# Kernel tuning notes

Measured on AMD Instinct MI355X. Metric: run time of the kernel, lower is better.

The kernel has to match this reference:

```python
import jax, jax.numpy as jnp
import numpy as np

M = 0.25
GAMMA = 256.0
HARD_W = 2.0
O_P = 1.0 + M
O_N = -M
DELTA_P = 1.0 - M
DELTA_N = M
NEG_BIG = -1e30  # masked-out fill for logsumexp (finite to keep grads NaN-free)


def setup_inputs() -> dict:
    key = jax.random.key(0)
    k1, k2 = jax.random.split(key)
    inputs = jax.random.normal(k1, (4096, 512), dtype=jnp.float32)
    targets = jax.random.randint(k2, (4096,), 0, 64, dtype=jnp.int64)
    return {"inputs": inputs, "targets": targets}


def reference(inputs, targets):
    n = inputs.shape[0]
    x = inputs / jnp.linalg.norm(inputs, axis=1, keepdims=True)  # L2 normalize
    sim = x @ x.T                                                # [n, n]

    same = targets[:, None] == targets[None, :]
    eye = jnp.eye(n, dtype=bool)
    pos_mask = same & ~eye
    neg_mask = ~same
    npos = pos_mask.sum(axis=1)
    nneg = neg_mask.sum(axis=1)

    sim_d = jax.lax.stop_gradient(sim)  # alphas are detached in the original
    alpha_p = jax.nn.relu(O_P - sim_d)
    alpha_n = jax.nn.relu(sim_d - O_N)

    # hard mining: scale alpha at hardest positive (min sim) / hardest negative (max sim)
    idx = jnp.arange(n)
    hard_p = jnp.argmin(jnp.where(pos_mask, sim_d, jnp.inf), axis=1)
    hard_n = jnp.argmax(jnp.where(neg_mask, sim_d, -jnp.inf), axis=1)
    hit_p = (idx[None, :] == hard_p[:, None]) & (npos > 1)[:, None]
    hit_n = (idx[None, :] == hard_n[:, None]) & (nneg > 1)[:, None]
    alpha_p = alpha_p * jnp.where(hit_p, HARD_W, 1.0)
    alpha_n = alpha_n * jnp.where(hit_n, HARD_W, 1.0)

    pos_term = jnp.where(pos_mask, -GAMMA * alpha_p * (sim - DELTA_P), NEG_BIG)
    neg_term = jnp.where(neg_mask, GAMMA * alpha_n * (sim - DELTA_N), NEG_BIG)
    lse_p = jax.nn.logsumexp(pos_term, axis=1)
    lse_n = jax.nn.logsumexp(neg_term, axis=1)

    valid = (npos > 0) & (nneg > 0)
    per_row = jnp.where(valid, jax.nn.softplus(lse_p + lse_n), 0.0)
    n_valid = jnp.maximum(valid.sum(), 1)
    return per_row.sum() / n_valid.astype(per_row.dtype)
```

## Files before the change

kernel.cpp:

```cpp
#include <hip/hip_runtime.h>


#define GAMMA_ 256.0f
#define MASKT_  (-1.0e4f)
#define MINITP_ (-1.0e4f)
#define MASKP_  (-3.0e4f)

constexpr int N_ = 4096;
constexpr int D_ = 512;
constexpr int AST_ = 520;
constexpr int CCH_ = 16;

typedef __bf16 bf16x8 __attribute__((ext_vector_type(8)));
typedef float  f32x4  __attribute__((ext_vector_type(4)));
typedef const unsigned int __attribute__((address_space(1)))* gp_t;
typedef unsigned int       __attribute__((address_space(3)))* lp_t;

__device__ __forceinline__ float pos_q(float s) {
    float d = s - 1.0f;
    return fmaf(d * d, 256.0f, -16.0f);
}
__device__ __forceinline__ float neg_q(float s) {
    float q = fmaf(s * s, 256.0f, -16.0f);
    return (s >= -0.25f) ? q : 0.0f;
}
__device__ __forceinline__ void lse_merge(float m2, float S2, float& m, float& S) {
    float mm = fmaxf(m, m2);
    S = S * __expf(m - mm) + S2 * __expf(m2 - mm);
    m = mm;
}
__device__ __forceinline__ unsigned short f2bf(float f) {
    unsigned int u = __float_as_uint(f);
    unsigned int r = u + 0x7FFFu + ((u >> 16) & 1u);
    return (unsigned short)(r >> 16);
}

__global__ __launch_bounds__(256) void k_norm(const float* __restrict__ in,
                                              unsigned short* __restrict__ xb,
                                              float* __restrict__ acc) {
    const int row  = blockIdx.x * 4 + (threadIdx.x >> 6);
    const int lane = threadIdx.x & 63;
    const float4* src = (const float4*)(in + (size_t)row * D_) + lane * 2;
    float4 a = src[0], b = src[1];
    float ss = a.x*a.x + a.y*a.y + a.z*a.z + a.w*a.w
             + b.x*b.x + b.y*b.y + b.z*b.z + b.w*b.w;
    #pragma unroll
    for (int d = 32; d >= 1; d >>= 1) ss += __shfl_xor(ss, d);
    float rn = 1.0f / sqrtf(ss);
    float v[8] = {a.x, a.y, a.z, a.w, b.x, b.y, b.z, b.w};
    union { uint4 u; unsigned short us[8]; } pk;
    #pragma unroll
    for (int k = 0; k < 8; ++k) pk.us[k] = f2bf(v[k] * rn);
    *((uint4*)(xb + (size_t)row * D_) + lane) = pk.u;
    if (blockIdx.x == 0 && threadIdx.x < 4) acc[threadIdx.x] = 0.0f;
}

__global__ __launch_bounds__(256, 4) void k_mainG(const unsigned short* __restrict__ xb,
                                                  const int* __restrict__ tg,
                                                  float* __restrict__ part) {
    constexpr int NST = 16;
    __shared__ __align__(16) unsigned short Bs[2][16][AST_];

    const int tid  = threadIdx.x;
    const int wave = tid >> 6, lane = tid & 63;
    const int n16  = lane & 15, quad = lane >> 4;
    const int rg   = (int)blockIdx.x >> 4;
    const int cc   = (int)blockIdx.x & 15;
    const int rowBase = rg * 64 + wave * 16;
    const int colBase = cc * 256;

    bf16x8 af[16];
    {
        const bf16x8* ap = (const bf16x8*)(xb + (size_t)(rowBase + n16) * D_ + quad * 8);
        #pragma unroll
        for (int kk = 0; kk < 16; ++kk) af[kk] = ap[kk * 4];
    }
    int tr[4];
    #pragma unroll
    for (int r = 0; r < 4; ++r) tr[r] = tg[rowBase + quad * 4 + r];

    float m_p[4], S_p[4], m_n[4], S_n[4], mxn[4];
    #pragma unroll
    for (int r = 0; r < 4; ++r) {
        m_p[r] = MINITP_; S_p[r] = 0.f; m_n[r] = 0.f; S_n[r] = 0.f; mxn[r] = -2.0f;
    }

    const char* gstage = (const char*)xb + (size_t)colBase * 1024 + lane * 16;

    #pragma unroll
    for (int p = 0; p < 4; ++p) {
        int j = p * 4 + wave;
        __builtin_amdgcn_global_load_lds((gp_t)(const void*)(gstage + j * 1024),
                                         (lp_t)(void*)&Bs[0][j][0], 16, 0, 0);
    }
    int tc_cur = tg[colBase + n16];

    auto epi = [&](const f32x4& a0, const f32x4& a1, int tcv, bool withDiag) {
        #pragma unroll
        for (int r = 0; r < 4; ++r) {
            float sim = a0[r] + a1[r];
            bool samec = (tr[r] == tcv);
            float u = samec ? (sim - 1.0f) : sim;
            float t = fmaf(u * u, 256.0f, -16.0f);
            if (!samec && sim < -0.25f) t = 0.0f;
            if (withDiag && n16 == quad * 4 + r) t = MASKP_;
            float ms = samec ? m_p[r] : m_n[r];
            if (t > ms) {
                float scl = __expf(ms - t);
                if (samec) { S_p[r] = fmaf(S_p[r], scl, 1.0f); m_p[r] = t; }
                else       { S_n[r] = fmaf(S_n[r], scl, 1.0f); m_n[r] = t; }
            } else {
                float e = __expf(t - ms);
                S_p[r] += samec ? e : 0.0f;
                S_n[r] += samec ? 0.0f : e;
            }
            mxn[r] = fmaxf(mxn[r], samec ? -2.0f : sim);
        }
    };

    #pragma unroll 1
    for (int s = 0; s < NST; ++s) {
        const int b = s & 1;
        const int j0 = colBase + s * 16;
        __syncthreads();

        if (s + 1 < NST) {
            const char* g2 = gstage + (size_t)(s + 1) * 16 * 1024;
            #pragma unroll
            for (int p = 0; p < 4; ++p) {
                int j = p * 4 + wave;
                __builtin_amdgcn_global_load_lds((gp_t)(const void*)(g2 + j * 1024),
                                                 (lp_t)(void*)&Bs[b ^ 1][j][0], 16, 0, 0);
            }
        }
        int tc_nxt = (s + 1 < NST) ? tg[colBase + (s + 1) * 16 + n16] : 0;

        f32x4 a0 = {0.f, 0.f, 0.f, 0.f}, a1 = {0.f, 0.f, 0.f, 0.f};
        #pragma unroll
        for (int kk = 0; kk < 8; ++kk) {
            bf16x8 bf0 = *(const bf16x8*)&Bs[b][n16][(2 * kk) * 32 + quad * 8];
            bf16x8 bf1 = *(const bf16x8*)&Bs[b][n16][(2 * kk + 1) * 32 + quad * 8];
            a0 = __builtin_amdgcn_mfma_f32_16x16x32_bf16(af[2 * kk],     bf0, a0, 0, 0, 0);
            a1 = __builtin_amdgcn_mfma_f32_16x16x32_bf16(af[2 * kk + 1], bf1, a1, 0, 0, 0);
        }

        if (j0 == rowBase) epi(a0, a1, tc_cur, true);
        else               epi(a0, a1, tc_cur, false);
        tc_cur = tc_nxt;
    }

    #pragma unroll
    for (int r = 0; r < 4; ++r) {
        #pragma unroll
        for (int d = 1; d <= 8; d <<= 1) {
            lse_merge(__shfl_xor(m_p[r], d), __shfl_xor(S_p[r], d), m_p[r], S_p[r]);
            lse_merge(__shfl_xor(m_n[r], d), __shfl_xor(S_n[r], d), m_n[r], S_n[r]);
            mxn[r] = fmaxf(mxn[r], __shfl_xor(mxn[r], d));
        }
    }
    if (n16 == 0) {
        #pragma unroll
        for (int r = 0; r < 4; ++r) {
            ((float4*)part)[(size_t)(rowBase + quad * 4 + r) * CCH_ + cc] =
                make_float4(m_p[r], S_p[r], mxn[r], S_n[r]);
        }
    }
}

__global__ __launch_bounds__(256) void k_reduceF(const float* __restrict__ part,
                                                 const int* __restrict__ tg,
                                                 float* __restrict__ acc,
                                                 float* __restrict__ out) {
    __shared__ int hist[64];
    const int tid = threadIdx.x;
    if (tid < 64) hist[tid] = 0;
    __syncthreads();
    for (int i = tid; i < N_; i += 256) atomicAdd(&hist[tg[i]], 1);
    __syncthreads();

    const int row = blockIdx.x * 256 + tid;
    const float4* P = (const float4*)part + (size_t)row * CCH_;
    float M_p = MINITP_, Sp = 0.f, M_n = 0.f, Sn = 0.f, mxn = -2.0f;
    #pragma unroll
    for (int c = 0; c < CCH_; ++c) {
        float4 a = P[c];
        lse_merge(a.x, a.y, M_p, Sp);
        float mn = (a.z > -1.5f) ? fmaxf(neg_q(a.z), 0.0f) : 0.0f;
        lse_merge(mn, a.w, M_n, Sn);
        mxn = fmaxf(mxn, a.z);
    }
    const int cnt = hist[tg[row]];
    float np2 = (float)(cnt - 1), nn2 = (float)(N_ - cnt);
    float loss = 0.f, vld = 0.f;
    if (np2 > 0.5f && nn2 > 0.5f) {
        if (np2 > 1.5f) {
            float t1 = M_p, t2 = 2.0f * t1;
            float mm = fmaxf(M_p, t2);
            Sp = Sp * __expf(M_p - mm) + __expf(t2 - mm) - __expf(t1 - mm);
            M_p = mm;
        }
        if (nn2 > 1.5f) {
            float t1 = neg_q(mxn), t2 = 2.0f * t1;
            float mm = fmaxf(M_n, t2);
            Sn = Sn * __expf(M_n - mm) + __expf(t2 - mm) - __expf(t1 - mm);
            M_n = mm;
        }
        float z = (M_p + __logf(Sp)) + (M_n + __logf(Sn));
        loss = fmaxf(z, 0.0f) + log1pf(__expf(-fabsf(z)));
        vld = 1.0f;
    }
    #pragma unroll
    for (int d = 32; d >= 1; d >>= 1) { loss += __shfl_xor(loss, d); vld += __shfl_xor(vld, d); }
    if ((tid & 63) == 0) { atomicAdd(&acc[0], loss); atomicAdd(&acc[1], vld); }

    __syncthreads();
    if (tid == 0) {
        __threadfence();
        int old = atomicAdd((int*)(acc + 2), 1);
        if (old == (int)gridDim.x - 1) {
            float ls = atomicAdd(&acc[0], 0.0f);
            float lv = atomicAdd(&acc[1], 0.0f);
            out[0] = ls / fmaxf(lv, 1.0f);
        }
    }
}

__global__ void k_final(const float* __restrict__ acc, float* __restrict__ out) {
    if (threadIdx.x == 0) out[0] = acc[0] / fmaxf(acc[1], 1.0f);
}

__global__ void k_sentinel(float* __restrict__ out) {
    if (threadIdx.x == 0) out[0] = -12345.0f;
}

__global__ __launch_bounds__(1024, 4) void k_main3(const unsigned short* __restrict__ xb,
                                                   const int* __restrict__ tg,
                                                   float* __restrict__ acc_g) {
    __shared__ __align__(16) unsigned short As[16 * AST_];
    __shared__ float sm[16][16][8];
    const int tid  = threadIdx.x;
    const int wave = tid >> 6, lane = tid & 63;
    const int n16  = lane & 15, quad = lane >> 4;
    const int rowBase = blockIdx.x * 16;
    {
        int row = tid >> 6, c = tid & 63;
        *(uint4*)&As[row * AST_ + c * 8] =
            *(const uint4*)(xb + (size_t)(rowBase + row) * D_ + c * 8);
    }
    int ir[4], tr[4];
    #pragma unroll
    for (int r = 0; r < 4; ++r) { ir[r] = rowBase + quad * 4 + r; tr[r] = tg[ir[r]]; }
    float m_p[4], S_p[4], m_n[4], S_n[4], mnp[4], mxn[4], sc[4];
    #pragma unroll
    for (int r = 0; r < 4; ++r) {
        m_p[r] = 0.f; S_p[r] = 0.f; m_n[r] = 0.f; S_n[r] = 0.f;
        mnp[r] = 2.0f; mxn[r] = -2.0f; sc[r] = 0.f;
    }
    __syncthreads();
    const unsigned short* Af = &As[n16 * AST_ + quad * 8];
    #pragma unroll 1
    for (int t = wave; t < N_ / 16; t += 16) {
        const int jcol = t * 16 + n16;
        const int tc = tg[jcol];
        const bf16x8* bp = (const bf16x8*)(xb + (size_t)jcol * D_ + quad * 8);
        bf16x8 bf[16];
        #pragma unroll
        for (int kk = 0; kk < 16; ++kk) bf[kk] = bp[kk * 4];
        f32x4 a0 = {0.f, 0.f, 0.f, 0.f}, a1 = {0.f, 0.f, 0.f, 0.f};
        #pragma unroll
        for (int kk = 0; kk < 8; ++kk) {
            bf16x8 af0 = *(const bf16x8*)(Af + (2 * kk) * 32);
            bf16x8 af1 = *(const bf16x8*)(Af + (2 * kk + 1) * 32);
            a0 = __builtin_amdgcn_mfma_f32_16x16x32_bf16(af0, bf[2 * kk],     a0, 0, 0, 0);
            a1 = __builtin_amdgcn_mfma_f32_16x16x32_bf16(af1, bf[2 * kk + 1], a1, 0, 0, 0);
        }
        #pragma unroll
        for (int r = 0; r < 4; ++r) {
            float s = a0[r] + a1[r];
            bool samec = (tr[r] == tc);
            bool posm  = samec && (jcol != ir[r]);
            float tp = posm  ? pos_q(s) : MASKT_;
            float tn = samec ? MASKT_ : neg_q(s);
            float mm = fmaxf(m_p[r], tp);
            S_p[r] = S_p[r] * __expf(m_p[r] - mm) + __expf(tp - mm); m_p[r] = mm;
            mm = fmaxf(m_n[r], tn);
            S_n[r] = S_n[r] * __expf(m_n[r] - mm) + __expf(tn - mm); m_n[r] = mm;
            sc[r] += samec ? 1.0f : 0.0f;
            mnp[r] = fminf(mnp[r], posm ? s : 2.0f);
            mxn[r] = fmaxf(mxn[r], samec ? -2.0f : s);
        }
    }
    #pragma unroll
    for (int r = 0; r < 4; ++r) {
        #pragma unroll
        for (int d = 1; d <= 8; d <<= 1) {
            lse_merge(__shfl_xor(m_p[r], d), __shfl_xor(S_p[r], d), m_p[r], S_p[r]);
            lse_merge(__shfl_xor(m_n[r], d), __shfl_xor(S_n[r], d), m_n[r], S_n[r]);
            mnp[r] = fminf(mnp[r], __shfl_xor(mnp[r], d));
            mxn[r] = fmaxf(mxn[r], __shfl_xor(mxn[r], d));
            sc[r] += __shfl_xor(sc[r], d);
        }
    }
    if (n16 == 0) {
        #pragma unroll
        for (int r = 0; r < 4; ++r) {
            float* q = sm[wave][quad * 4 + r];
            q[0] = m_p[r]; q[1] = S_p[r]; q[2] = m_n[r]; q[3] = S_n[r];
            q[4] = mnp[r]; q[5] = mxn[r]; q[6] = sc[r];
        }
    }
    __syncthreads();
    if (tid < 64) {
        const int L = tid & 15;
        float m_p2 = 0.f, S_p2 = 0.f, m_n2 = 0.f, S_n2 = 0.f;
        float mnp2 = 2.0f, mxn2 = -2.0f, sct = 0.f;
        #pragma unroll
        for (int w = 0; w < 16; ++w) {
            const float* q = sm[w][L];
            lse_merge(q[0], q[1], m_p2, S_p2);
            lse_merge(q[2], q[3], m_n2, S_n2);
            mnp2 = fminf(mnp2, q[4]); mxn2 = fmaxf(mxn2, q[5]);
            sct += q[6];
        }
        float loss = 0.f, vld = 0.f;
        float np2 = sct - 1.0f, nn2 = (float)N_ - sct;
        if (tid < 16 && np2 > 0.5f && nn2 > 0.5f) {
            if (np2 > 1.5f) {
                float t1 = pos_q(mnp2), t2 = 2.0f * t1;
                float mm = fmaxf(m_p2, t2);
                S_p2 = S_p2 * __expf(m_p2 - mm) + __expf(t2 - mm) - __expf(t1 - mm);
                m_p2 = mm;
            }
            if (nn2 > 1.5f) {
                float t1 = neg_q(mxn2), t2 = 2.0f * t1;
                float mm = fmaxf(m_n2, t2);
                S_n2 = S_n2 * __expf(m_n2 - mm) + __expf(t2 - mm) - __expf(t1 - mm);
                m_n2 = mm;
            }
            float z = (m_p2 + __logf(S_p2)) + (m_n2 + __logf(S_n2));
            loss = fmaxf(z, 0.0f) + log1pf(__expf(-fabsf(z)));
            vld = 1.0f;
        }
        #pragma unroll
        for (int d = 32; d >= 1; d >>= 1) {
            loss += __shfl_xor(loss, d); vld += __shfl_xor(vld, d);
        }
        if (tid == 0) { atomicAdd(&acc_g[0], loss); atomicAdd(&acc_g[1], vld); }
    }
}

extern "C" void kernel_launch(void* const* d_in, const int* in_sizes, int n_in,
                              void* d_out, int out_size, void* d_ws, size_t ws_size,
                              hipStream_t stream) {
    const float* in = (const float*)d_in[0];
    const int*   tg = (const int*)d_in[1];
    constexpr size_t MB = 1024 * 1024;
    unsigned short* xb = (unsigned short*)d_ws;

    if (ws_size >= 5 * MB + 64) {
        float* part = (float*)((char*)d_ws + 4 * MB);
        float* acc  = (float*)((char*)d_ws + 5 * MB);
        hipLaunchKernelGGL(k_norm,    dim3(N_ / 4),    dim3(256), 0, stream, in, xb, acc);
        hipLaunchKernelGGL(k_mainG,   dim3(64 * CCH_), dim3(256), 0, stream, xb, tg, part);
        hipLaunchKernelGGL(k_reduceF, dim3(N_ / 256),  dim3(256), 0, stream, part, tg, acc,
                           (float*)d_out);
    } else if (ws_size >= 4 * MB + 64) {
        float* acc = (float*)((char*)d_ws + 4 * MB);
        hipLaunchKernelGGL(k_norm,  dim3(N_ / 4),  dim3(256),  0, stream, in, xb, acc);
        hipLaunchKernelGGL(k_main3, dim3(N_ / 16), dim3(1024), 0, stream, xb, tg, acc);
        hipLaunchKernelGGL(k_final, dim3(1),       dim3(64),   0, stream, acc, (float*)d_out);
    } else {
        hipLaunchKernelGGL(k_sentinel, dim3(1), dim3(64), 0, stream, (float*)d_out);
    }
}
```

Before: 104.9 us.

## Exploit Gram symmetry with triangular tiles and per-class positive kernel

Adds a new path that computes only the upper-triangular 256-column tiles of the similarity matrix (544 blocks instead of 1024), using each tile for both row-wise and column-wise negative logsumexp partials written to a column buffer. Positive terms move to a separate per-class kernel that gathers rows of each class and computes only same-class similarities. A new reduction merges the row partials, column partials and positive partials. This is meant to roughly halve the MFMA and epilogue work, at the cost of an extra kernel launch, a large column-partials buffer (8 MB) with its extra writes and reads, and an assumption that each class has at most 128 members.

```diff
diff --git a/kernel.cpp b/kernel.cpp
--- a/kernel.cpp
+++ b/kernel.cpp
@@ -1,7 +1,6 @@
 #include <hip/hip_runtime.h>
 
 
-#define GAMMA_ 256.0f
 #define MASKT_  (-1.0e4f)
 #define MINITP_ (-1.0e4f)
 #define MASKP_  (-3.0e4f)
@@ -55,12 +54,299 @@
     if (blockIdx.x == 0 && threadIdx.x < 4) acc[threadIdx.x] = 0.0f;
 }
 
+__global__ __launch_bounds__(256) void k_pos(const unsigned short* __restrict__ xb,
+                                             const int* __restrict__ tg,
+                                             float* __restrict__ posp) {
+    __shared__ int list[128];
+    __shared__ int cntS;
+    __shared__ __align__(16) unsigned short Bs[2][16][AST_];
+    const int tid  = threadIdx.x;
+    const int cls  = (int)blockIdx.x >> 1;
+    const int half = (int)blockIdx.x & 1;
+    if (tid == 0) cntS = 0;
+    __syncthreads();
+    for (int i = tid; i < N_; i += 256)
+        if (tg[i] == cls) { int p = atomicAdd(&cntS, 1); if (p < 128) list[p] = i; }
+    __syncthreads();
+    const int mc = min(cntS, 128);
+    if (mc == 0) return;
+    if (half == 1 && mc <= 64) return;
+
+    const int wave = tid >> 6, lane = tid & 63;
+    const int n16  = lane & 15, quad = lane >> 4;
+    const int rt   = half * 4 + wave;
+    const int nst  = (mc + 15) >> 4;
+
+    const int arow = list[min(rt * 16 + n16, mc - 1)];
+    bf16x8 af[16];
+    {
+        const bf16x8* ap = (const bf16x8*)(xb + (size_t)arow * D_ + quad * 8);
+        #pragma unroll
+        for (int kk = 0; kk < 16; ++kk) af[kk] = ap[kk * 4];
+    }
+    int ir[4];
+    #pragma unroll
+    for (int r = 0; r < 4; ++r) {
+        int idx = rt * 16 + quad * 4 + r;
+        ir[r] = (idx < mc) ? list[idx] : -2;
+    }
+    float m[4], S[4], mnp[4];
+    #pragma unroll
+    for (int r = 0; r < 4; ++r) { m[r] = MINITP_; S[r] = 0.f; mnp[r] = 2.f; }
+
+    #pragma unroll
+    for (int p = 0; p < 4; ++p) {
+        int jj = p * 4 + wave;
+        int gi = list[min(jj, mc - 1)];
+        __builtin_amdgcn_global_load_lds(
+            (gp_t)(const void*)((const char*)xb + (size_t)gi * 1024 + lane * 16),
+            (lp_t)(void*)&Bs[0][jj][0], 16, 0, 0);
+    }
+    int jg = (n16 < mc) ? list[n16] : -1;
+
+    #pragma unroll 1
+    for (int s = 0; s < nst; ++s) {
+        const int b = s & 1;
+        __syncthreads();
+        if (s + 1 < nst) {
+            #pragma unroll
+            for (int p = 0; p < 4; ++p) {
+                int jj = p * 4 + wave;
+                int gi = list[min((s + 1) * 16 + jj, mc - 1)];
+                __builtin_amdgcn_global_load_lds(
+                    (gp_t)(const void*)((const char*)xb + (size_t)gi * 1024 + lane * 16),
+                    (lp_t)(void*)&Bs[b ^ 1][jj][0], 16, 0, 0);
+            }
+        }
+        int jg_nxt = (s + 1 < nst && ((s + 1) * 16 + n16) < mc) ? list[(s + 1) * 16 + n16] : -1;
+
+        f32x4 a0 = {0.f,0.f,0.f,0.f}, a1 = {0.f,0.f,0.f,0.f};
+        #pragma unroll
+        for (int kk = 0; kk < 8; ++kk) {
+            bf16x8 bf0 = *(const bf16x8*)&Bs[b][n16][(2 * kk) * 32 + quad * 8];
+            bf16x8 bf1 = *(const bf16x8*)&Bs[b][n16][(2 * kk + 1) * 32 + quad * 8];
+            a0 = __builtin_amdgcn_mfma_f32_16x16x32_bf16(af[2 * kk],     bf0, a0, 0, 0, 0);
+            a1 = __builtin_amdgcn_mfma_f32_16x16x32_bf16(af[2 * kk + 1], bf1, a1, 0, 0, 0);
+        }
+        #pragma unroll
+        for (int r = 0; r < 4; ++r) {
+            float sim = a0[r] + a1[r];
+            bool live = (jg >= 0) && (ir[r] >= 0) && (jg != ir[r]);
+            float t = live ? pos_q(sim) : MASKP_;
+            if (t > m[r]) { float scl = __expf(m[r] - t); S[r] = fmaf(S[r], scl, 1.f); m[r] = t; }
+            else          { S[r] += __expf(t - m[r]); }
+            mnp[r] = fminf(mnp[r], live ? sim : 2.f);
+        }
+        jg = jg_nxt;
+    }
+    #pragma unroll
+    for (int r = 0; r < 4; ++r) {
+        #pragma unroll
+        for (int d = 1; d <= 8; d <<= 1) {
+            lse_merge(__shfl_xor(m[r], d), __shfl_xor(S[r], d), m[r], S[r]);
+            mnp[r] = fminf(mnp[r], __shfl_xor(mnp[r], d));
+        }
+    }
+    if (n16 == 0) {
+        #pragma unroll
+        for (int r = 0; r < 4; ++r)
+            if (ir[r] >= 0)
+                ((float4*)posp)[ir[r]] = make_float4(m[r], S[r], mnp[r], (float)(mc - 1));
+    }
+}
+
+__global__ __launch_bounds__(256, 4) void k_mainS(const unsigned short* __restrict__ xb,
+                                                  const int* __restrict__ tg,
+                                                  float* __restrict__ rowp,
+                                                  float* __restrict__ colp) {
+    constexpr int NST = 16;
+    __shared__ __align__(16) unsigned short Bs[2][16][AST_];
+    const int tid  = threadIdx.x;
+    const int wave = tid >> 6, lane = tid & 63;
+    const int n16  = lane & 15, quad = lane >> 4;
+
+    const int bid = (int)blockIdx.x;
+    int cc = (int)((sqrtf((float)(1 + 2 * bid)) - 1.0f) * 0.5f);
+    while (2 * (cc + 1) * (cc + 2) <= bid) ++cc;
+    while (2 * cc * (cc + 1) > bid) --cc;
+    const int rg = bid - 2 * cc * (cc + 1);
+    const bool above = (rg < 4 * cc);
+    const int rowBase = rg * 64 + wave * 16;
+    const int colBase = cc * 256;
+
+    bf16x8 af[16];
+    {
+        const bf16x8* ap = (const bf16x8*)(xb + (size_t)(rowBase + n16) * D_ + quad * 8);
+        #pragma unroll
+        for (int kk = 0; kk < 16; ++kk) af[kk] = ap[kk * 4];
+    }
+    int tr[4];
+    #pragma unroll
+    for (int r = 0; r < 4; ++r) tr[r] = tg[rowBase + quad * 4 + r];
+
+    float m[4], S[4], mexp[4], mxn[4];
+    #pragma unroll
+    for (int r = 0; r < 4; ++r) { m[r] = 0.f; S[r] = 0.f; mexp[r] = 1.f; mxn[r] = -2.f; }
+
+    const char* gstage = (const char*)xb + (size_t)colBase * 1024 + lane * 16;
+    #pragma unroll
+    for (int p = 0; p < 4; ++p) {
+        int j = p * 4 + wave;
+        __builtin_amdgcn_global_load_lds((gp_t)(const void*)(gstage + j * 1024),
+                                         (lp_t)(void*)&Bs[0][j][0], 16, 0, 0);
+    }
+    int tc_cur = tg[colBase + n16];
+
+    #pragma unroll 1
+    for (int s = 0; s < NST; ++s) {
+        const int b = s & 1;
+        __syncthreads();
+        if (s + 1 < NST) {
+            const char* g2 = gstage + (size_t)(s + 1) * 16 * 1024;
+            #pragma unroll
+            for (int p = 0; p < 4; ++p) {
+                int j = p * 4 + wave;
+                __builtin_amdgcn_global_load_lds((gp_t)(const void*)(g2 + j * 1024),
+                                                 (lp_t)(void*)&Bs[b ^ 1][j][0], 16, 0, 0);
+            }
+        }
+        int tc_nxt = (s + 1 < NST) ? tg[colBase + (s + 1) * 16 + n16] : 0;
+
+        f32x4 a0 = {0.f,0.f,0.f,0.f}, a1 = {0.f,0.f,0.f,0.f};
+        #pragma unroll
+        for (int kk = 0; kk < 8; ++kk) {
+            bf16x8 bf0 = *(const bf16x8*)&Bs[b][n16][(2 * kk) * 32 + quad * 8];
+            bf16x8 bf1 = *(const bf16x8*)&Bs[b][n16][(2 * kk + 1) * 32 + quad * 8];
+            a0 = __builtin_amdgcn_mfma_f32_16x16x32_bf16(af[2 * kk],     bf0, a0, 0, 0, 0);
+            a1 = __builtin_amdgcn_mfma_f32_16x16x32_bf16(af[2 * kk + 1], bf1, a1, 0, 0, 0);
+        }
+
+        float cs = 0.f, cm = -2.f;
+        #pragma unroll
+        for (int r = 0; r < 4; ++r) {
+            float sim = a0[r] + a1[r];
+            bool samec = (tr[r] == tc_cur);
+            float t = fmaf(sim * sim, 256.f, -16.f);
+            if (sim < -0.25f) t = 0.f;
+            float ms = m[r];
+            if (!samec && t > ms) {
+                float scl = __expf(ms - t);
+                S[r] = fmaf(S[r], scl, 1.f);
+                m[r] = t; mexp[r] = __expf(t);
+                cs += mexp[r];
+            } else {
+                float e  = __expf(t - ms);
+                float en = samec ? 0.f : e;
+                S[r] += en;
+                cs = fmaf(en, mexp[r], cs);
+            }
+            float sn = samec ? -2.f : sim;
+            mxn[r] = fmaxf(mxn[r], sn);
+            cm = fmaxf(cm, sn);
+        }
+        if (above) {
+            cs += __shfl_xor(cs, 16); cs += __shfl_xor(cs, 32);
+            cm = fmaxf(cm, __shfl_xor(cm, 16)); cm = fmaxf(cm, __shfl_xor(cm, 32));
+            if (lane < 16) {
+                float im = (cm > 0.25f) ? fmaf(cm * cm, 256.f, -16.f) : 0.f;
+                int jcol = colBase + (s << 4) + lane;
+                int wrow = rg * 4 + wave;
+                ((float2*)colp)[(size_t)wrow * N_ + jcol] =
+                    make_float2(cm, cs * __expf(-im));
+            }
+        }
+        tc_cur = tc_nxt;
+    }
+
+    #pragma unroll
+    for (int r = 0; r < 4; ++r) {
+        #pragma unroll
+        for (int d = 1; d <= 8; d <<= 1) {
+            lse_merge(__shfl_xor(m[r], d), __shfl_xor(S[r], d), m[r], S[r]);
+            mxn[r] = fmaxf(mxn[r], __shfl_xor(mxn[r], d));
+        }
+    }
+    if (n16 == 0) {
+        #pragma unroll
+        for (int r = 0; r < 4; ++r)
+            ((float2*)rowp)[(size_t)cc * N_ + rowBase + quad * 4 + r] =
+                make_float2(mxn[r], S[r]);
+    }
+}
+
+__device__ __forceinline__ void merge_neg(float mx, float Sp, float& M, float& S, float& mxn) {
+    if (mx > -1.5f) {
+        float im = (mx > 0.25f) ? fmaf(mx * mx, 256.f, -16.f) : 0.f;
+        lse_merge(im, Sp, M, S);
+        mxn = fmaxf(mxn, mx);
+    }
+}
+__global__ __launch_bounds__(256) void k_reduceS(const float* __restrict__ rowp,
+                                                 const float* __restrict__ colp,
+                                                 const float* __restrict__ posp,
+                                                 float* __restrict__ acc,
+                                                 float* __restrict__ out) {
+    const int tid = threadIdx.x;
+    const int j   = blockIdx.x * 256 + tid;
+    const int ccj = j >> 8;
+    float M = 0.f, S = 0.f, mxn = -2.f;
+    for (int cc = ccj; cc < 16; ++cc) {
+        float2 a = ((const float2*)rowp)[(size_t)cc * N_ + j];
+        merge_neg(a.x, a.y, M, S, mxn);
+    }
+    const int wmax = ccj << 4;
+    for (int w = 0; w < wmax; ++w) {
+        float2 a = ((const float2*)colp)[(size_t)w * N_ + j];
+        merge_neg(a.x, a.y, M, S, mxn);
+    }
+    float4 pp = ((const float4*)posp)[j];
+    float M_p = pp.x, Sp = pp.y;
+    float np2 = pp.w, nn2 = 4095.f - pp.w;
+    float loss = 0.f, vld = 0.f;
+    if (np2 > 0.5f && nn2 > 0.5f) {
+        if (np2 > 1.5f) {
+            float t1 = M_p, t2 = 2.f * t1;
+            float mm = fmaxf(M_p, t2);
+            Sp = Sp * __expf(M_p - mm) + __expf(t2 - mm) - __expf(t1 - mm);
+            M_p = mm;
+        }
+        if (nn2 > 1.5f) {
+            float t1 = neg_q(mxn), t2 = 2.f * t1;
+            float mm = fmaxf(M, t2);
+            S = S * __expf(M - mm) + __expf(t2 - mm) - __expf(t1 - mm);
+            M = mm;
+        }
+        float z = (M_p + __logf(Sp)) + (M + __logf(S));
+        loss = fmaxf(z, 0.f) + log1pf(__expf(-fabsf(z)));
+        vld = 1.f;
+    }
+    #pragma unroll
+    for (int d = 32; d >= 1; d >>= 1) { loss += __shfl_xor(loss, d); vld += __shfl_xor(vld, d); }
+    if ((tid & 63) == 0) { atomicAdd(&acc[0], loss); atomicAdd(&acc[1], vld); }
+    __syncthreads();
+    if (tid == 0) {
+        __threadfence();
+        int old = atomicAdd((int*)(acc + 2), 1);
+        if (old == (int)gridDim.x - 1) {
+            float ls = atomicAdd(&acc[0], 0.f);
+            float lv = atomicAdd(&acc[1], 0.f);
+            out[0] = ls / fmaxf(lv, 1.f);
+        }
+    }
+}
+
+__global__ void k_final(const float* __restrict__ acc, float* __restrict__ out) {
+    if (threadIdx.x == 0) out[0] = acc[0] / fmaxf(acc[1], 1.0f);
+}
+__global__ void k_sentinel(float* __restrict__ out) {
+    if (threadIdx.x == 0) out[0] = -12345.0f;
+}
+
 __global__ __launch_bounds__(256, 4) void k_mainG(const unsigned short* __restrict__ xb,
                                                   const int* __restrict__ tg,
                                                   float* __restrict__ part) {
     constexpr int NST = 16;
     __shared__ __align__(16) unsigned short Bs[2][16][AST_];
-
     const int tid  = threadIdx.x;
     const int wave = tid >> 6, lane = tid & 63;
     const int n16  = lane & 15, quad = lane >> 4;
@@ -68,7 +354,6 @@
     const int cc   = (int)blockIdx.x & 15;
     const int rowBase = rg * 64 + wave * 16;
     const int colBase = cc * 256;
-
     bf16x8 af[16];
     {
         const bf16x8* ap = (const bf16x8*)(xb + (size_t)(rowBase + n16) * D_ + quad * 8);
@@ -78,15 +363,12 @@
     int tr[4];
     #pragma unroll
     for (int r = 0; r < 4; ++r) tr[r] = tg[rowBase + quad * 4 + r];
-
     float m_p[4], S_p[4], m_n[4], S_n[4], mxn[4];
     #pragma unroll
     for (int r = 0; r < 4; ++r) {
         m_p[r] = MINITP_; S_p[r] = 0.f; m_n[r] = 0.f; S_n[r] = 0.f; mxn[r] = -2.0f;
     }
-
     const char* gstage = (const char*)xb + (size_t)colBase * 1024 + lane * 16;
-
     #pragma unroll
     for (int p = 0; p < 4; ++p) {
         int j = p * 4 + wave;
@@ -94,7 +376,6 @@
                                          (lp_t)(void*)&Bs[0][j][0], 16, 0, 0);
     }
     int tc_cur = tg[colBase + n16];
-
     auto epi = [&](const f32x4& a0, const f32x4& a1, int tcv, bool withDiag) {
         #pragma unroll
         for (int r = 0; r < 4; ++r) {
@@ -117,13 +398,11 @@
             mxn[r] = fmaxf(mxn[r], samec ? -2.0f : sim);
         }
     };
-
     #pragma unroll 1
     for (int s = 0; s < NST; ++s) {
         const int b = s & 1;
         const int j0 = colBase + s * 16;
         __syncthreads();
-
         if (s + 1 < NST) {
             const char* g2 = gstage + (size_t)(s + 1) * 16 * 1024;
             #pragma unroll
@@ -134,8 +413,7 @@
             }
         }
         int tc_nxt = (s + 1 < NST) ? tg[colBase + (s + 1) * 16 + n16] : 0;
-
-        f32x4 a0 = {0.f, 0.f, 0.f, 0.f}, a1 = {0.f, 0.f, 0.f, 0.f};
+        f32x4 a0 = {0.f,0.f,0.f,0.f}, a1 = {0.f,0.f,0.f,0.f};
         #pragma unroll
         for (int kk = 0; kk < 8; ++kk) {
             bf16x8 bf0 = *(const bf16x8*)&Bs[b][n16][(2 * kk) * 32 + quad * 8];
@@ -143,12 +421,10 @@
             a0 = __builtin_amdgcn_mfma_f32_16x16x32_bf16(af[2 * kk],     bf0, a0, 0, 0, 0);
             a1 = __builtin_amdgcn_mfma_f32_16x16x32_bf16(af[2 * kk + 1], bf1, a1, 0, 0, 0);
         }
-
         if (j0 == rowBase) epi(a0, a1, tc_cur, true);
         else               epi(a0, a1, tc_cur, false);
         tc_cur = tc_nxt;
     }
-
     #pragma unroll
     for (int r = 0; r < 4; ++r) {
         #pragma unroll
@@ -160,10 +436,9 @@
     }
     if (n16 == 0) {
         #pragma unroll
-        for (int r = 0; r < 4; ++r) {
+        for (int r = 0; r < 4; ++r)
             ((float4*)part)[(size_t)(rowBase + quad * 4 + r) * CCH_ + cc] =
                 make_float4(m_p[r], S_p[r], mxn[r], S_n[r]);
-        }
     }
 }
 
@@ -177,7 +452,6 @@
     __syncthreads();
     for (int i = tid; i < N_; i += 256) atomicAdd(&hist[tg[i]], 1);
     __syncthreads();
-
     const int row = blockIdx.x * 256 + tid;
     const float4* P = (const float4*)part + (size_t)row * CCH_;
     float M_p = MINITP_, Sp = 0.f, M_n = 0.f, Sn = 0.f, mxn = -2.0f;
@@ -212,7 +486,6 @@
     #pragma unroll
     for (int d = 32; d >= 1; d >>= 1) { loss += __shfl_xor(loss, d); vld += __shfl_xor(vld, d); }
     if ((tid & 63) == 0) { atomicAdd(&acc[0], loss); atomicAdd(&acc[1], vld); }
-
     __syncthreads();
     if (tid == 0) {
         __threadfence();
@@ -223,14 +496,6 @@
             out[0] = ls / fmaxf(lv, 1.0f);
         }
     }
-}
-
-__global__ void k_final(const float* __restrict__ acc, float* __restrict__ out) {
-    if (threadIdx.x == 0) out[0] = acc[0] / fmaxf(acc[1], 1.0f);
-}
-
-__global__ void k_sentinel(float* __restrict__ out) {
-    if (threadIdx.x == 0) out[0] = -12345.0f;
 }
 
 __global__ __launch_bounds__(1024, 4) void k_main3(const unsigned short* __restrict__ xb,
@@ -266,7 +531,7 @@
         bf16x8 bf[16];
         #pragma unroll
         for (int kk = 0; kk < 16; ++kk) bf[kk] = bp[kk * 4];
-        f32x4 a0 = {0.f, 0.f, 0.f, 0.f}, a1 = {0.f, 0.f, 0.f, 0.f};
+        f32x4 a0 = {0.f,0.f,0.f,0.f}, a1 = {0.f,0.f,0.f,0.f};
         #pragma unroll
         for (int kk = 0; kk < 8; ++kk) {
             bf16x8 af0 = *(const bf16x8*)(Af + (2 * kk) * 32);
@@ -357,7 +622,17 @@
     constexpr size_t MB = 1024 * 1024;
     unsigned short* xb = (unsigned short*)d_ws;
 
-    if (ws_size >= 5 * MB + 64) {
+    if (ws_size >= 13 * MB + 65536 + 64) {
+        float* rowp = (float*)((char*)d_ws + 4 * MB);
+        float* colp = (float*)((char*)d_ws + 5 * MB);
+        float* posp = (float*)((char*)d_ws + 13 * MB);
+        float* acc  = (float*)((char*)d_ws + 13 * MB + 65536);
+        hipLaunchKernelGGL(k_norm,    dim3(N_ / 4),   dim3(256), 0, stream, in, xb, acc);
+        hipLaunchKernelGGL(k_pos,     dim3(128),      dim3(256), 0, stream, xb, tg, posp);
+        hipLaunchKernelGGL(k_mainS,   dim3(544),      dim3(256), 0, stream, xb, tg, rowp, colp);
+        hipLaunchKernelGGL(k_reduceS, dim3(N_ / 256), dim3(256), 0, stream, rowp, colp, posp,
+                           acc, (float*)d_out);
+    } else if (ws_size >= 5 * MB + 64) {
         float* part = (float*)((char*)d_ws + 4 * MB);
         float* acc  = (float*)((char*)d_ws + 5 * MB);
         hipLaunchKernelGGL(k_norm,    dim3(N_ / 4),    dim3(256), 0, stream, in, xb, acc);
```

Result: slower. 188.8 us (+79.9%).
